# Kernel tuning notes

Hardware: AMD Instinct MI355X
Metric: run time of the kernel (lower is better)

Reference implementation:

```python
import jax, jax.numpy as jnp
import numpy as np

N = 100000
EPS = 1e-5
NEG_SLOPE = 0.2


def gat_conv(x, src, dst, W, a_src, a_dst, b):
    # x: [N, din]; W: [dout, din]; a_src/a_dst/b: [dout]
    h = x @ W.T                              # [N, dout]
    alpha_s = h @ a_src                      # [N]
    alpha_d = h @ a_dst                      # [N]
    e = jax.nn.leaky_relu(alpha_s[src] + alpha_d[dst], NEG_SLOPE)  # [E]
    # segment softmax over incoming edges of each destination node
    emax = jax.ops.segment_max(e, dst, num_segments=N)
    ex = jnp.exp(e - emax[dst])
    denom = jax.ops.segment_sum(ex, dst, num_segments=N)
    alpha = ex / denom[dst]                  # [E]
    out = jax.ops.segment_sum(alpha[:, None] * h[src], dst, num_segments=N)
    return out + b


def batch_norm(x, gamma, beta):
    mu = jnp.mean(x, axis=0)
    var = jnp.var(x, axis=0)
    return gamma * (x - mu) * jax.lax.rsqrt(var + EPS) + beta


def setup_inputs() -> dict:
    key = jax.random.key(0)
    ks = jax.random.split(key, 20)
    din, dh, dout = 128, 128, 128
    E = 1600000
    x = jax.random.normal(ks[0], (N, din), dtype=jnp.float32)
    edge_index = jax.random.randint(ks[1], (2, E), 0, N, dtype=jnp.int32)
    def glorot(k, shape):
        fan = sum(shape)
        s = jnp.sqrt(6.0 / fan)
        return jax.random.uniform(k, shape, dtype=jnp.float32, minval=-s, maxval=s)
    inp = {"x": x, "edge_index": edge_index}
    dims = [(din, dh), (dh, dh), (dh, dout)]
    for l, (di, do) in enumerate(dims):
        inp[f"W{l}"] = glorot(ks[2 + 4 * l], (do, di))
        inp[f"a_src{l}"] = glorot(ks[3 + 4 * l], (do,)) * 0.1
        inp[f"a_dst{l}"] = glorot(ks[4 + 4 * l], (do,)) * 0.1
        inp[f"b{l}"] = jnp.zeros((do,), dtype=jnp.float32)
    for l in range(2):
        inp[f"gamma{l}"] = jnp.ones((dh,), dtype=jnp.float32)
        inp[f"beta{l}"] = jnp.zeros((dh,), dtype=jnp.float32)
    return inp


def reference(x, edge_index, W0, a_src0, a_dst0, b0, W1, a_src1, a_dst1, b1,
              W2, a_src2, a_dst2, b2, gamma0, beta0, gamma1, beta1):
    # add self-loops (PyG GATConv default)
    ar = jnp.arange(N, dtype=edge_index.dtype)
    src = jnp.concatenate([edge_index[0], ar])
    dst = jnp.concatenate([edge_index[1], ar])
    h = gat_conv(x, src, dst, W0, a_src0, a_dst0, b0)
    h = jax.nn.relu(batch_norm(h, gamma0, beta0))
    h = gat_conv(h, src, dst, W1, a_src1, a_dst1, b1)
    h = jax.nn.relu(batch_norm(h, gamma1, beta1))
    out = gat_conv(h, src, dst, W2, a_src2, a_dst2, b2)
    return out
```

## Files before the change

### kernel.cpp

```cpp
#include <hip/hip_runtime.h>
#include <cstdint>
#include <cstddef>

#define NN 100000
#define NP 100096
#define EE 1600000
#define ET 1700000
#define NBKT 196
#define TILE 2048
#define STAT_BLOCKS 400

typedef short  bf16x8 __attribute__((ext_vector_type(8)));
typedef float  f32x4  __attribute__((ext_vector_type(4)));

__device__ __forceinline__ unsigned short f2bf(float f) {
    unsigned int x = __builtin_bit_cast(unsigned int, f);
    x += 0x7FFFu + ((x >> 16) & 1u);
    return (unsigned short)(x >> 16);
}
__device__ __forceinline__ unsigned int pk2(float lo, float hi) {
    return ((unsigned int)f2bf(hi) << 16) | (unsigned int)f2bf(lo);
}
__device__ __forceinline__ float bflo(unsigned int u) {
    return __builtin_bit_cast(float, u << 16);
}
__device__ __forceinline__ float bfhi(unsigned int u) {
    return __builtin_bit_cast(float, u & 0xFFFF0000u);
}
__device__ __forceinline__ int unperm(int j) { return ((j & 7) << 4) | (j >> 3); }


__global__ void k_bcount(const int* __restrict__ ei, int* __restrict__ btot) {
    __shared__ int h[256];
    int t = threadIdx.x;
    h[t] = 0;
    __syncthreads();
    for (int e = blockIdx.x * 256 + t; e < ET; e += 256 * 256) {
        int d = (e < EE) ? ei[EE + e] : (e - EE);
        atomicAdd(&h[d >> 9], 1);
    }
    __syncthreads();
    if (h[t]) atomicAdd(&btot[t], h[t]);
}

__global__ void k_bscan(const int* __restrict__ btot, int* __restrict__ bstart,
                        int* __restrict__ bcur, int* __restrict__ off) {
    __shared__ int s[256];
    int t = threadIdx.x;
    int v = (t < NBKT) ? btot[t] : 0;
    s[t] = v;
    __syncthreads();
    for (int o = 1; o < 256; o <<= 1) {
        int a = (t >= o) ? s[t - o] : 0;
        __syncthreads();
        s[t] += a;
        __syncthreads();
    }
    int ex = s[t] - v;
    if (t <= NBKT) bstart[t] = (t < NBKT) ? ex : ET;
    if (t == NBKT - 1) bstart[NBKT] = s[t];
    bcur[t] = ex;
    if (t == 0) off[NN] = ET;
}

__global__ __launch_bounds__(256) void k_bucket(
    const int* __restrict__ ei, int* __restrict__ bcur, unsigned int* __restrict__ bucketed)
{
    __shared__ int h4[4][256], woff[4][256], loff[256], gbase[256], sc[256];
    __shared__ unsigned int stage[TILE];
    __shared__ int gaddr[TILE];
    __shared__ int stot_s;
    const int t = threadIdx.x;
    const int w = t >> 6;
    const int e0 = blockIdx.x * TILE;

    h4[0][t] = 0; h4[1][t] = 0; h4[2][t] = 0; h4[3][t] = 0;
    __syncthreads();

    unsigned int pk[TILE / 256];
    int bk[TILE / 256];
#pragma unroll
    for (int i = 0; i < TILE / 256; ++i) {
        int e = e0 + i * 256 + t;
        bk[i] = -1;
        if (e < ET) {
            int s, d;
            if (e < EE) { s = ei[e]; d = ei[EE + e]; } else { s = e - EE; d = s; }
            bk[i] = d >> 9;
            pk[i] = ((unsigned int)(d & 511) << 17) | (unsigned int)s;
            atomicAdd(&h4[w][bk[i]], 1);
        }
    }
    __syncthreads();

    int h0 = h4[0][t], h1 = h4[1][t], h2 = h4[2][t], h3 = h4[3][t];
    int tot = h0 + h1 + h2 + h3;
    sc[t] = tot;
    __syncthreads();
    for (int o = 1; o < 256; o <<= 1) {
        int a = (t >= o) ? sc[t - o] : 0;
        __syncthreads();
        sc[t] += a;
        __syncthreads();
    }
    int lo = sc[t] - tot;
    loff[t] = lo;
    woff[0][t] = lo;
    woff[1][t] = lo + h0;
    woff[2][t] = lo + h0 + h1;
    woff[3][t] = lo + h0 + h1 + h2;
    if (t < NBKT && tot) gbase[t] = atomicAdd(&bcur[t], tot);
    if (t == 255) stot_s = sc[255];
    h4[0][t] = 0; h4[1][t] = 0; h4[2][t] = 0; h4[3][t] = 0;
    __syncthreads();

#pragma unroll
    for (int i = 0; i < TILE / 256; ++i) {
        if (bk[i] >= 0) {
            int b = bk[i];
            int r = woff[w][b] + atomicAdd(&h4[w][b], 1);
            stage[r] = pk[i];
            gaddr[r] = gbase[b] + (r - loff[b]);
        }
    }
    __syncthreads();

    const int stot = stot_s;
    for (int j = t; j < stot; j += 256)
        bucketed[gaddr[j]] = stage[j];
}

__global__ __launch_bounds__(256) void k_csr(
    const unsigned int* __restrict__ bucketed, const int* __restrict__ bstart,
    int* __restrict__ off, int* __restrict__ srcs)
{
    __shared__ int h[512], sc2[512], c2[512], sp[256];
    const int t = threadIdx.x;
    const int b = blockIdx.x;
    const int beg = bstart[b], end = bstart[b + 1];
    const int cnt = end - beg;

    h[t] = 0; h[t + 256] = 0; c2[t] = 0; c2[t + 256] = 0;
    __syncthreads();
    for (int i = t; i < cnt; i += 256)
        atomicAdd(&h[bucketed[beg + i] >> 17], 1);
    __syncthreads();

    int a0 = h[2 * t], a1 = h[2 * t + 1];
    sp[t] = a0 + a1;
    __syncthreads();
    for (int o = 1; o < 256; o <<= 1) {
        int a = (t >= o) ? sp[t - o] : 0;
        __syncthreads();
        sp[t] += a;
        __syncthreads();
    }
    int ep = sp[t] - (a0 + a1);
    sc2[2 * t] = ep;
    sc2[2 * t + 1] = ep + a0;
    __syncthreads();

    const int d0 = b << 9;
#pragma unroll
    for (int k = t; k < 512; k += 256) {
        int d = d0 + k;
        if (d < NN) off[d] = beg + sc2[k];
    }

    for (int i = t; i < cnt; i += 256) {
        unsigned int v = bucketed[beg + i];
        int ld = v >> 17;
        int r = atomicAdd(&c2[ld], 1);
        srcs[beg + sc2[ld] + r] = (int)(v & 0x1FFFFu);
    }
}

__global__ void k_cvtw3(const float* __restrict__ W0, const float* __restrict__ W1,
                        const float* __restrict__ W2, unsigned short* __restrict__ Wb) {
    int i = blockIdx.x * 256 + threadIdx.x;
    int layer = i >> 14;
    const float* W = (layer == 0) ? W0 : (layer == 1) ? W1 : W2;
    int base = i & 16383;
    int src = (layer == 0) ? base : ((base & ~127) | unperm(base & 127));
    Wb[i] = f2bf(W[src]);
}

template<int MODE>
__global__ __launch_bounds__(256) void k_mfma(
    const void* __restrict__ Xv, const unsigned short* __restrict__ Wb,
    const float* __restrict__ gsum, const float* __restrict__ gsq,
    const float* __restrict__ gamma, const float* __restrict__ beta,
    const float* __restrict__ asrc, const float* __restrict__ adst,
    unsigned short* __restrict__ Hb, float* __restrict__ AS, float* __restrict__ AD)
{
    __shared__ float scale_s[128], shift_s[128];
    const int t    = threadIdx.x;
    const int lane = t & 63;
    const int c    = lane & 15;
    const int q    = lane >> 4;
    const int r0   = blockIdx.x * 64 + (t >> 6) * 16;
    const int row  = r0 + c;

    if (MODE) {
        if (t < 128) {
            int ot = unperm(t);
            float mu  = gsum[t] * (1.f / NN);
            float var = gsq[t] * (1.f / NN) - mu * mu;
            float sc  = gamma[ot] * rsqrtf(var + 1e-5f);
            scale_s[t] = sc;
            shift_s[t] = beta[ot] - mu * sc;
        }
        __syncthreads();
    }

    union { uint4 u; bf16x8 v; } Af[4];
    if (row < NN) {
        if (MODE) {
            const unsigned short* xp = (const unsigned short*)Xv + ((size_t)row << 7) + (q << 3);
#pragma unroll
            for (int k0 = 0; k0 < 4; ++k0) {
                uint4 r = *(const uint4*)(xp + (k0 << 5));
                const int kb = (k0 << 5) + (q << 3);
                float a0 = bflo(r.x), a1 = bfhi(r.x), a2 = bflo(r.y), a3 = bfhi(r.y);
                float a4 = bflo(r.z), a5 = bfhi(r.z), a6 = bflo(r.w), a7 = bfhi(r.w);
                float4 sA = *(const float4*)&scale_s[kb];
                float4 sB = *(const float4*)&scale_s[kb + 4];
                float4 hA = *(const float4*)&shift_s[kb];
                float4 hB = *(const float4*)&shift_s[kb + 4];
                a0 = fmaxf(0.f, fmaf(a0, sA.x, hA.x));
                a1 = fmaxf(0.f, fmaf(a1, sA.y, hA.y));
                a2 = fmaxf(0.f, fmaf(a2, sA.z, hA.z));
                a3 = fmaxf(0.f, fmaf(a3, sA.w, hA.w));
                a4 = fmaxf(0.f, fmaf(a4, sB.x, hB.x));
                a5 = fmaxf(0.f, fmaf(a5, sB.y, hB.y));
                a6 = fmaxf(0.f, fmaf(a6, sB.z, hB.z));
                a7 = fmaxf(0.f, fmaf(a7, sB.w, hB.w));
                Af[k0].u.x = pk2(a0, a1);
                Af[k0].u.y = pk2(a2, a3);
                Af[k0].u.z = pk2(a4, a5);
                Af[k0].u.w = pk2(a6, a7);
            }
        } else {
            const float* xp = (const float*)Xv + ((size_t)row << 7) + (q << 3);
#pragma unroll
            for (int k0 = 0; k0 < 4; ++k0) {
                float4 a = *(const float4*)(xp + (k0 << 5));
                float4 b = *(const float4*)(xp + (k0 << 5) + 4);
                Af[k0].u.x = pk2(a.x, a.y);
                Af[k0].u.y = pk2(a.z, a.w);
                Af[k0].u.z = pk2(b.x, b.y);
                Af[k0].u.w = pk2(b.z, b.w);
            }
        }
    } else {
#pragma unroll
        for (int k0 = 0; k0 < 4; ++k0) Af[k0].u = make_uint4(0, 0, 0, 0);
    }

    f32x4 acc[8];
#pragma unroll
    for (int nt = 0; nt < 8; ++nt) acc[nt] = (f32x4){0.f, 0.f, 0.f, 0.f};

#pragma unroll
    for (int nt = 0; nt < 8; ++nt) {
        union { uint4 u; bf16x8 v; } Bf[4];
        const size_t bbase = ((size_t)(nt * 16 + c) << 7) + (q << 3);
#pragma unroll
        for (int k0 = 0; k0 < 4; ++k0)
            Bf[k0].u = *(const uint4*)(Wb + bbase + (k0 << 5));
#pragma unroll
        for (int k0 = 0; k0 < 4; ++k0)
            acc[nt] = __builtin_amdgcn_mfma_f32_16x16x32_bf16(Af[k0].v, Bf[k0].v, acc[nt], 0, 0, 0);
    }

    float ps[4] = {0.f, 0.f, 0.f, 0.f}, pd[4] = {0.f, 0.f, 0.f, 0.f};
#pragma unroll
    for (int nt = 0; nt < 8; ++nt) {
        float av = asrc[nt * 16 + c];
        float dv = adst[nt * 16 + c];
#pragma unroll
        for (int r = 0; r < 4; ++r) {
            ps[r] = fmaf(acc[nt][r], av, ps[r]);
            pd[r] = fmaf(acc[nt][r], dv, pd[r]);
        }
    }
#pragma unroll
    for (int m = 1; m < 16; m <<= 1) {
#pragma unroll
        for (int r = 0; r < 4; ++r) { ps[r] += __shfl_xor(ps[r], m); pd[r] += __shfl_xor(pd[r], m); }
    }
    if (c == 0) {
#pragma unroll
        for (int r = 0; r < 4; ++r) {
            int grow = r0 + q * 4 + r;
            if (grow < NN) { AS[grow] = ps[r]; AD[grow] = pd[r]; }
        }
    }

#pragma unroll
    for (int r = 0; r < 4; ++r) {
        int grow = r0 + q * 4 + r;
        if (grow < NN) {
            uint4 o;
            o.x = pk2(acc[0][r], acc[1][r]);
            o.y = pk2(acc[2][r], acc[3][r]);
            o.z = pk2(acc[4][r], acc[5][r]);
            o.w = pk2(acc[6][r], acc[7][r]);
            *(uint4*)(Hb + ((size_t)grow << 7) + (c << 3)) = o;
        }
    }
}

template<int OUTBF>
__global__ __launch_bounds__(256) void k_agg(
    const int* __restrict__ off, const int* __restrict__ srcs,
    const unsigned short* __restrict__ Hb, const float* __restrict__ AS,
    const float* __restrict__ AD, const float* __restrict__ bias,
    void* __restrict__ OUT)
{
    __shared__ uint2 s_e[4][64];
    const int wid  = threadIdx.x >> 6;
    const int lane = threadIdx.x & 63;
    const int g    = lane >> 4;
    const int x16  = lane & 15;
    const int n    = blockIdx.x * 4 + wid;
    const int beg = off[n], end = off[n + 1];
    const float adn = AD[n];

    float acc[8];
#pragma unroll
    for (int i = 0; i < 8; ++i) acc[i] = 0.f;
    float den = 0.f;

    for (int base = beg; base < end; base += 64) {
        int cnt = end - base; if (cnt > 64) cnt = 64;
        float wgt = 0.f; int s = 0;
        if (lane < cnt) {
            s = srcs[base + lane];
            float e = AS[s] + adn;
            e = (e > 0.f) ? e : 0.2f * e;
            wgt = __expf(e);
        }
        s_e[wid][lane] = make_uint2((unsigned int)s, __builtin_bit_cast(unsigned int, wgt));
        den += wgt;
        int rounds = (cnt + 3) >> 2;
        for (int j = 0; j < rounds; ++j) {
            uint2 ew = s_e[wid][(j << 2) + g];
            float wq = __builtin_bit_cast(float, ew.y);
            uint4 u = *((const uint4*)(Hb + ((size_t)ew.x << 7)) + x16);
            acc[0] = fmaf(wq, bflo(u.x), acc[0]);
            acc[1] = fmaf(wq, bfhi(u.x), acc[1]);
            acc[2] = fmaf(wq, bflo(u.y), acc[2]);
            acc[3] = fmaf(wq, bfhi(u.y), acc[3]);
            acc[4] = fmaf(wq, bflo(u.z), acc[4]);
            acc[5] = fmaf(wq, bfhi(u.z), acc[5]);
            acc[6] = fmaf(wq, bflo(u.w), acc[6]);
            acc[7] = fmaf(wq, bfhi(u.w), acc[7]);
        }
    }

#pragma unroll
    for (int i = 0; i < 8; ++i) {
        acc[i] += __shfl_xor(acc[i], 16);
        acc[i] += __shfl_xor(acc[i], 32);
    }
#pragma unroll
    for (int o = 32; o; o >>= 1) den += __shfl_xor(den, o);
    float inv = 1.f / den;

    if (g == 0) {
        float o8[8];
#pragma unroll
        for (int i = 0; i < 8; ++i)
            o8[i] = fmaf(acc[i], inv, bias[i * 16 + x16]);
        if (OUTBF) {
            uint4 pkd;
            pkd.x = pk2(o8[0], o8[1]); pkd.y = pk2(o8[2], o8[3]);
            pkd.z = pk2(o8[4], o8[5]); pkd.w = pk2(o8[6], o8[7]);
            *(uint4*)((unsigned short*)OUT + ((size_t)n << 7) + (x16 << 3)) = pkd;
        } else {
            float* op = (float*)OUT + ((size_t)n << 7) + x16;
#pragma unroll
            for (int i = 0; i < 8; ++i)
                op[i * 16] = o8[i];
        }
    }
}

__global__ __launch_bounds__(256) void k_colsum(const unsigned int* __restrict__ Xb,
                                                float* __restrict__ gsum, float* __restrict__ gsq) {
    __shared__ float ls[4][128], lq[4][128];
    const int t = threadIdx.x;
    const int c2 = t & 63;
    const int half = t >> 6;
    float s0 = 0.f, s1 = 0.f, q0 = 0.f, q1 = 0.f;
    for (int r = blockIdx.x * 4 + half; r < NN; r += STAT_BLOCKS * 4) {
        unsigned int v = Xb[(size_t)r * 64 + c2];
        float f0 = bflo(v), f1 = bfhi(v);
        s0 += f0; q0 += f0 * f0;
        s1 += f1; q1 += f1 * f1;
    }
    ls[half][2 * c2] = s0; ls[half][2 * c2 + 1] = s1;
    lq[half][2 * c2] = q0; lq[half][2 * c2 + 1] = q1;
    __syncthreads();
    if (t < 128) {
        float ss = ls[0][t] + ls[1][t] + ls[2][t] + ls[3][t];
        float qq = lq[0][t] + lq[1][t] + lq[2][t] + lq[3][t];
        atomicAdd(&gsum[t], ss);
        atomicAdd(&gsq[t], qq);
    }
}

extern "C" void kernel_launch(void* const* d_in, const int* in_sizes, int n_in,
                              void* d_out, int out_size, void* d_ws, size_t ws_size,
                              hipStream_t stream)
{
    const float* x  = (const float*)d_in[0];
    const int*   ei = (const int*)d_in[1];
    const float* Wm[3]  = {(const float*)d_in[2], (const float*)d_in[6],  (const float*)d_in[10]};
    const float* Asr[3] = {(const float*)d_in[3], (const float*)d_in[7],  (const float*)d_in[11]};
    const float* Ads[3] = {(const float*)d_in[4], (const float*)d_in[8],  (const float*)d_in[12]};
    const float* Bs[3]  = {(const float*)d_in[5], (const float*)d_in[9],  (const float*)d_in[13]};
    const float* gam[2] = {(const float*)d_in[14], (const float*)d_in[16]};
    const float* bet[2] = {(const float*)d_in[15], (const float*)d_in[17]};

    char* p = (char*)d_ws;
    auto carve = [&](size_t bytes) -> char* {
        char* r = p;
        p += (bytes + 255) & ~(size_t)255;
        return r;
    };
    int*   off_   = (int*)carve((size_t)(NN + 1) * 4);
    int*   srcs   = (int*)carve((size_t)ET * 4);
    unsigned int* bucketed = (unsigned int*)carve((size_t)ET * 4);
    int*   btot   = (int*)carve(256 * 4);
    float* gstat  = (float*)carve(4 * 128 * 4);
    int*   bstart = (int*)carve(260 * 4);
    int*   bcur   = (int*)carve(256 * 4);
    unsigned short* Hb  = (unsigned short*)carve((size_t)NP * 128 * 2);
    unsigned short* Wb  = (unsigned short*)carve((size_t)3 * 16384 * 2);
    float* AS    = (float*)carve((size_t)NN * 4);
    float* AD    = (float*)carve((size_t)NN * 4);

    float*          OUTf = (float*)d_out;
    unsigned short* OUTb = (unsigned short*)d_out;

    (void)hipMemsetAsync(btot, 0, 256 * 4 + 4 * 128 * 4, stream);

    k_bcount<<<256, 256, 0, stream>>>(ei, btot);
    k_bscan<<<1, 256, 0, stream>>>(btot, bstart, bcur, off_);
    k_bucket<<<(ET + TILE - 1) / TILE, 256, 0, stream>>>(ei, bcur, bucketed);
    k_csr<<<NBKT, 256, 0, stream>>>(bucketed, bstart, off_, srcs);

    k_cvtw3<<<192, 256, 0, stream>>>(Wm[0], Wm[1], Wm[2], Wb);

    const int MFMA_GRID = NP / 64;

    k_mfma<0><<<MFMA_GRID, 256, 0, stream>>>(x, Wb, nullptr, nullptr, nullptr, nullptr,
                                             Asr[0], Ads[0], Hb, AS, AD);
    k_agg<1><<<NN / 4, 256, 0, stream>>>(off_, srcs, Hb, AS, AD, Bs[0], OUTb);
    k_colsum<<<STAT_BLOCKS, 256, 0, stream>>>((const unsigned int*)OUTb, gstat, gstat + 128);

    k_mfma<1><<<MFMA_GRID, 256, 0, stream>>>(OUTb, Wb + 16384, gstat, gstat + 128,
                                             gam[0], bet[0], Asr[1], Ads[1], Hb, AS, AD);
    k_agg<1><<<NN / 4, 256, 0, stream>>>(off_, srcs, Hb, AS, AD, Bs[1], OUTb);
    k_colsum<<<STAT_BLOCKS, 256, 0, stream>>>((const unsigned int*)OUTb, gstat + 256, gstat + 384);

    k_mfma<1><<<MFMA_GRID, 256, 0, stream>>>(OUTb, Wb + 32768, gstat + 256, gstat + 384,
                                             gam[1], bet[1], Asr[2], Ads[2], Hb, AS, AD);
    k_agg<0><<<NN / 4, 256, 0, stream>>>(off_, srcs, Hb, AS, AD, Bs[2], OUTf);
}
```

Before: 535.0 us.

## Fuse batchnorm statistics into aggregation epilogue and merge preprocessing kernels

Column sum and sum-of-squares for batch norm are now accumulated inside the aggregation kernel from the values it writes, using shared-memory reduction and atomics spread over 8 slots, removing the separate colsum passes over the activations. The bucket-count and weight conversion kernels are merged into one launch, and weights are stored pre-swizzled in MFMA fragment order so B loads are contiguous per lane. This trades extra reread traffic and launches for many global atomics from every aggregation block.

Measured after the change: 487.4 us. 8.9% less time.

```diff
diff --git a/kernel.cpp b/kernel.cpp
--- a/kernel.cpp
+++ b/kernel.cpp
@@ -8,7 +8,7 @@
 #define ET 1700000
 #define NBKT 196
 #define TILE 2048
-#define STAT_BLOCKS 400
+#define NSLOT 8
 
 typedef short  bf16x8 __attribute__((ext_vector_type(8)));
 typedef float  f32x4  __attribute__((ext_vector_type(4)));
@@ -29,18 +29,35 @@
 }
 __device__ __forceinline__ int unperm(int j) { return ((j & 7) << 4) | (j >> 3); }
 
-
-__global__ void k_bcount(const int* __restrict__ ei, int* __restrict__ btot) {
-    __shared__ int h[256];
-    int t = threadIdx.x;
-    h[t] = 0;
-    __syncthreads();
-    for (int e = blockIdx.x * 256 + t; e < ET; e += 256 * 256) {
-        int d = (e < EE) ? ei[EE + e] : (e - EE);
-        atomicAdd(&h[d >> 9], 1);
-    }
-    __syncthreads();
-    if (h[t]) atomicAdd(&btot[t], h[t]);
+__global__ void k_pre(const int* __restrict__ ei,
+                      const float* __restrict__ W0, const float* __restrict__ W1,
+                      const float* __restrict__ W2, unsigned short* __restrict__ Wb,
+                      int* __restrict__ btot)
+{
+    const int t = threadIdx.x;
+    const int b = blockIdx.x;
+    if (b < 256) {
+        __shared__ int h[256];
+        h[t] = 0;
+        __syncthreads();
+        for (int e = b * 256 + t; e < ET; e += 256 * 256) {
+            int d = (e < EE) ? ei[EE + e] : (e - EE);
+            atomicAdd(&h[d >> 9], 1);
+        }
+        __syncthreads();
+        if (h[t]) atomicAdd(&btot[t], h[t]);
+    } else {
+        int i = (b - 256) * 256 + t;
+        int layer = i >> 14;
+        const float* W = (layer == 0) ? W0 : (layer == 1) ? W1 : W2;
+        int o  = i & 16383;
+        int f  = o >> 3, e = o & 7;
+        int nt = f >> 8, k0 = (f >> 6) & 3, lane = f & 63;
+        int c  = lane & 15, q = lane >> 4;
+        int k  = k0 * 32 + q * 8 + e;
+        int col = (layer == 0) ? k : unperm(k);
+        Wb[i] = f2bf(W[(nt * 16 + c) * 128 + col]);
+    }
 }
 
 __global__ void k_bscan(const int* __restrict__ btot, int* __restrict__ bstart,
@@ -175,20 +192,10 @@
     }
 }
 
-__global__ void k_cvtw3(const float* __restrict__ W0, const float* __restrict__ W1,
-                        const float* __restrict__ W2, unsigned short* __restrict__ Wb) {
-    int i = blockIdx.x * 256 + threadIdx.x;
-    int layer = i >> 14;
-    const float* W = (layer == 0) ? W0 : (layer == 1) ? W1 : W2;
-    int base = i & 16383;
-    int src = (layer == 0) ? base : ((base & ~127) | unperm(base & 127));
-    Wb[i] = f2bf(W[src]);
-}
-
 template<int MODE>
 __global__ __launch_bounds__(256) void k_mfma(
     const void* __restrict__ Xv, const unsigned short* __restrict__ Wb,
-    const float* __restrict__ gsum, const float* __restrict__ gsq,
+    const float* __restrict__ gstat8,
     const float* __restrict__ gamma, const float* __restrict__ beta,
     const float* __restrict__ asrc, const float* __restrict__ adst,
     unsigned short* __restrict__ Hb, float* __restrict__ AS, float* __restrict__ AD)
@@ -203,9 +210,15 @@
 
     if (MODE) {
         if (t < 128) {
+            float su = 0.f, sq = 0.f;
+#pragma unroll
+            for (int s = 0; s < NSLOT; ++s) {
+                su += gstat8[s * 256 + t];
+                sq += gstat8[s * 256 + 128 + t];
+            }
             int ot = unperm(t);
-            float mu  = gsum[t] * (1.f / NN);
-            float var = gsq[t] * (1.f / NN) - mu * mu;
+            float mu  = su * (1.f / NN);
+            float var = sq * (1.f / NN) - mu * mu;
             float sc  = gamma[ot] * rsqrtf(var + 1e-5f);
             scale_s[t] = sc;
             shift_s[t] = beta[ot] - mu * sc;
@@ -264,10 +277,9 @@
 #pragma unroll
     for (int nt = 0; nt < 8; ++nt) {
         union { uint4 u; bf16x8 v; } Bf[4];
-        const size_t bbase = ((size_t)(nt * 16 + c) << 7) + (q << 3);
 #pragma unroll
         for (int k0 = 0; k0 < 4; ++k0)
-            Bf[k0].u = *(const uint4*)(Wb + bbase + (k0 << 5));
+            Bf[k0].u = *(const uint4*)(Wb + ((size_t)(((nt << 2) + k0) * 64 + lane) << 3));
 #pragma unroll
         for (int k0 = 0; k0 < 4; ++k0)
             acc[nt] = __builtin_amdgcn_mfma_f32_16x16x32_bf16(Af[k0].v, Bf[k0].v, acc[nt], 0, 0, 0);
@@ -316,9 +328,10 @@
     const int* __restrict__ off, const int* __restrict__ srcs,
     const unsigned short* __restrict__ Hb, const float* __restrict__ AS,
     const float* __restrict__ AD, const float* __restrict__ bias,
-    void* __restrict__ OUT)
+    void* __restrict__ OUT, float* __restrict__ gstat)
 {
     __shared__ uint2 s_e[4][64];
+    __shared__ float ssum[4][128], ssq[4][128];
     const int wid  = threadIdx.x >> 6;
     const int lane = threadIdx.x & 63;
     const int g    = lane >> 4;
@@ -378,6 +391,11 @@
             pkd.x = pk2(o8[0], o8[1]); pkd.y = pk2(o8[2], o8[3]);
             pkd.z = pk2(o8[4], o8[5]); pkd.w = pk2(o8[6], o8[7]);
             *(uint4*)((unsigned short*)OUT + ((size_t)n << 7) + (x16 << 3)) = pkd;
+#pragma unroll
+            for (int i = 0; i < 8; ++i) {
+                ssum[wid][(x16 << 3) + i] = o8[i];
+                ssq[wid][(x16 << 3) + i]  = o8[i] * o8[i];
+            }
         } else {
             float* op = (float*)OUT + ((size_t)n << 7) + x16;
 #pragma unroll
@@ -385,29 +403,17 @@
                 op[i * 16] = o8[i];
         }
     }
-}
-
-__global__ __launch_bounds__(256) void k_colsum(const unsigned int* __restrict__ Xb,
-                                                float* __restrict__ gsum, float* __restrict__ gsq) {
-    __shared__ float ls[4][128], lq[4][128];
-    const int t = threadIdx.x;
-    const int c2 = t & 63;
-    const int half = t >> 6;
-    float s0 = 0.f, s1 = 0.f, q0 = 0.f, q1 = 0.f;
-    for (int r = blockIdx.x * 4 + half; r < NN; r += STAT_BLOCKS * 4) {
-        unsigned int v = Xb[(size_t)r * 64 + c2];
-        float f0 = bflo(v), f1 = bfhi(v);
-        s0 += f0; q0 += f0 * f0;
-        s1 += f1; q1 += f1 * f1;
-    }
-    ls[half][2 * c2] = s0; ls[half][2 * c2 + 1] = s1;
-    lq[half][2 * c2] = q0; lq[half][2 * c2 + 1] = q1;
-    __syncthreads();
-    if (t < 128) {
-        float ss = ls[0][t] + ls[1][t] + ls[2][t] + ls[3][t];
-        float qq = lq[0][t] + lq[1][t] + lq[2][t] + lq[3][t];
-        atomicAdd(&gsum[t], ss);
-        atomicAdd(&gsq[t], qq);
+
+    if (OUTBF) {
+        __syncthreads();
+        const int t = threadIdx.x;
+        if (t < 128) {
+            float ss = ssum[0][t] + ssum[1][t] + ssum[2][t] + ssum[3][t];
+            float qq = ssq[0][t] + ssq[1][t] + ssq[2][t] + ssq[3][t];
+            float* gs = gstat + (blockIdx.x & (NSLOT - 1)) * 256;
+            atomicAdd(&gs[t], ss);
+            atomicAdd(&gs[128 + t], qq);
+        }
     }
 }
 
@@ -434,7 +440,7 @@
     int*   srcs   = (int*)carve((size_t)ET * 4);
     unsigned int* bucketed = (unsigned int*)carve((size_t)ET * 4);
     int*   btot   = (int*)carve(256 * 4);
-    float* gstat  = (float*)carve(4 * 128 * 4);
+    float* gstat  = (float*)carve(2 * NSLOT * 256 * 4);
     int*   bstart = (int*)carve(260 * 4);
     int*   bcur   = (int*)carve(256 * 4);
     unsigned short* Hb  = (unsigned short*)carve((size_t)NP * 128 * 2);
@@ -445,28 +451,25 @@
     float*          OUTf = (float*)d_out;
     unsigned short* OUTb = (unsigned short*)d_out;
 
-    (void)hipMemsetAsync(btot, 0, 256 * 4 + 4 * 128 * 4, stream);
-
-    k_bcount<<<256, 256, 0, stream>>>(ei, btot);
+    (void)hipMemsetAsync(btot, 0, 256 * 4 + 2 * NSLOT * 256 * 4, stream);
+
+    k_pre<<<448, 256, 0, stream>>>(ei, Wm[0], Wm[1], Wm[2], Wb, btot);
     k_bscan<<<1, 256, 0, stream>>>(btot, bstart, bcur, off_);
     k_bucket<<<(ET + TILE - 1) / TILE, 256, 0, stream>>>(ei, bcur, bucketed);
     k_csr<<<NBKT, 256, 0, stream>>>(bucketed, bstart, off_, srcs);
 
-    k_cvtw3<<<192, 256, 0, stream>>>(Wm[0], Wm[1], Wm[2], Wb);
-
     const int MFMA_GRID = NP / 64;
 
-    k_mfma<0><<<MFMA_GRID, 256, 0, stream>>>(x, Wb, nullptr, nullptr, nullptr, nullptr,
+    k_mfma<0><<<MFMA_GRID, 256, 0, stream>>>(x, Wb, nullptr, nullptr, nullptr,
                                              Asr[0], Ads[0], Hb, AS, AD);
-    k_agg<1><<<NN / 4, 256, 0, stream>>>(off_, srcs, Hb, AS, AD, Bs[0], OUTb);
-    k_colsum<<<STAT_BLOCKS, 256, 0, stream>>>((const unsigned int*)OUTb, gstat, gstat + 128);
-
-    k_mfma<1><<<MFMA_GRID, 256, 0, stream>>>(OUTb, Wb + 16384, gstat, gstat + 128,
+    k_agg<1><<<NN / 4, 256, 0, stream>>>(off_, srcs, Hb, AS, AD, Bs[0], OUTb, gstat);
+
+    k_mfma<1><<<MFMA_GRID, 256, 0, stream>>>(OUTb, Wb + 16384, gstat,
                                              gam[0], bet[0], Asr[1], Ads[1], Hb, AS, AD);
-    k_agg<1><<<NN / 4, 256, 0, stream>>>(off_, srcs, Hb, AS, AD, Bs[1], OUTb);
-    k_colsum<<<STAT_BLOCKS, 256, 0, stream>>>((const unsigned int*)OUTb, gstat + 256, gstat + 384);
-
-    k_mfma<1><<<MFMA_GRID, 256, 0, stream>>>(OUTb, Wb + 32768, gstat + 256, gstat + 384,
+    k_agg<1><<<NN / 4, 256, 0, stream>>>(off_, srcs, Hb, AS, AD, Bs[1], OUTb,
+                                         gstat + NSLOT * 256);
+
+    k_mfma<1><<<MFMA_GRID, 256, 0, stream>>>(OUTb, Wb + 32768, gstat + NSLOT * 256,
                                              gam[1], bet[1], Asr[2], Ads[2], Hb, AS, AD);
-    k_agg<0><<<NN / 4, 256, 0, stream>>>(off_, srcs, Hb, AS, AD, Bs[2], OUTf);
-}
+    k_agg<0><<<NN / 4, 256, 0, stream>>>(off_, srcs, Hb, AS, AD, Bs[2], OUTf, nullptr);
+}
```
